# Kernel optimization log

Hardware: AMD Instinct MI355X
Metric: run time of the kernel (lower is better)

Reference implementation:

```python
import jax, jax.numpy as jnp
import numpy as np

N, NFEAT, NHID, NCLASS, NLAYERS = 4096, 512, 512, 40, 3
NEG = -9e15


def _adj(key, p=0.01):
    # sparse binary adjacency with self-loops, matching the `adj > 0` masking
    a = (jax.random.uniform(key, (N, N)) < p).astype(jnp.float32)
    return jnp.minimum(a + jnp.eye(N, dtype=jnp.float32), 1.0)


def setup_inputs() -> dict:
    key = jax.random.key(0)
    ks = jax.random.split(key, 16)
    inp = {
        "x": jax.random.normal(ks[0], (N, NFEAT), jnp.float32),
        "adj_att": _adj(ks[1]),
        "adj1": _adj(ks[2]),
        "adj2": _adj(ks[3]),
        "hop_select": jnp.ones((NLAYERS,), jnp.float32),
    }
    s1 = 1.0 / np.sqrt(NFEAT)
    s2 = 1.0 / np.sqrt(NHID)
    for i in range(NLAYERS):
        inp[f"W_fc{i}"] = jax.random.uniform(ks[4 + i], (NFEAT, NHID), jnp.float32, -s1, s1)
        inp[f"b_fc{i}"] = jnp.zeros((NHID,), jnp.float32)
    for i in range(NLAYERS - 1):
        inp[f"W_q{i}"] = jax.random.uniform(ks[7 + 2 * i], (NHID, NHID), jnp.float32, -s2, s2)
        inp[f"b_q{i}"] = jnp.zeros((NHID,), jnp.float32)
        inp[f"W_k{i}"] = jax.random.uniform(ks[8 + 2 * i], (NHID, NHID), jnp.float32, -s2, s2)
        inp[f"b_k{i}"] = jnp.zeros((NHID,), jnp.float32)
    s3 = 1.0 / np.sqrt(NHID * NLAYERS)
    inp["W_cls"] = jax.random.uniform(ks[11], (NHID * NLAYERS, NCLASS), jnp.float32, -s3, s3)
    inp["b_cls"] = jnp.zeros((NCLASS,), jnp.float32)
    return inp


def _gatv3_forward(x, adj_att, adj1, adj2, hop_select,
                   W_fc0, b_fc0, W_fc1, b_fc1, W_fc2, b_fc2,
                   W_q0, b_q0, W_k0, b_k0, W_q1, b_q1, W_k1, b_k1,
                   W_cls, b_cls):
    mask = jax.nn.softmax(hop_select, axis=-1)
    adjs = [None, adj1, adj2]
    fc = [(W_fc0, b_fc0), (W_fc1, b_fc1), (W_fc2, b_fc2)]
    qk = [(W_q0, b_q0, W_k0, b_k0), (W_q1, b_q1, W_k1, b_k1)]
    outs = []
    tmp_1 = None
    for i in range(NLAYERS):
        W, b = fc[i]
        tmp = x @ W + b  # [N, nhid]
        if adjs[i] is not None:
            adj = adjs[i]
            Wq, bq, Wk, bk = qk[i - 1]
            t_att = adj_att @ tmp                      # [N, nhid]
            Q = adj_att @ (t_att @ Wq + bq)            # GCN1 Q, act=None
            K = adj_att @ (t_att @ Wk + bk)            # GCN1 K, act=None
            scores = jnp.where(adj > 0, Q @ K.T, NEG)  # masked QK^T
            att = jax.nn.softmax(scores, axis=-1)
            tmp_1 = jnp.where(adj > 0, att, 0.0)
            tmp = att @ tmp
        # F.normalize(p=2, dim=1) with eps=1e-12 clamp
        nrm = jnp.maximum(jnp.sqrt(jnp.sum(tmp * tmp, axis=1, keepdims=True)), 1e-12)
        outs.append(mask[i] * (tmp / nrm))
    final = jnp.concatenate(outs, axis=1)          # [N, 3*nhid]
    out = jax.nn.relu(final)                       # dropout is identity in eval
    logits = out @ W_cls + b_cls
    return jax.nn.log_softmax(logits, axis=1), tmp_1


def reference(x, adj_att, adj1, adj2, hop_select,
              W_fc0, b_fc0, W_fc1, b_fc1, W_fc2, b_fc2,
              W_q0, b_q0, W_k0, b_k0, W_q1, b_q1, W_k1, b_k1,
              W_cls, b_cls):
    return _gatv3_forward(x, adj_att, adj1, adj2, hop_select,
                          W_fc0, b_fc0, W_fc1, b_fc1, W_fc2, b_fc2,
                          W_q0, b_q0, W_k0, b_k0, W_q1, b_q1, W_k1, b_k1,
                          W_cls, b_cls)
```

## Files before the change

### kernel.cpp

```cpp
#include <hip/hip_runtime.h>
#include <math.h>

#define NN 4096
#define DD 512
#define ELL 128

typedef unsigned long long u64;
typedef __attribute__((ext_vector_type(8))) short short8;
typedef __attribute__((ext_vector_type(8))) unsigned short ushort8;
typedef __attribute__((ext_vector_type(4))) float f32x4;

static __device__ __forceinline__ unsigned short f2bf(float f) {
  unsigned u = __float_as_uint(f);
  unsigned r = (u + 0x7fffu + ((u >> 16) & 1u)) >> 16;
  return (unsigned short)r;
}
static __device__ __forceinline__ float bf2f(unsigned short h) {
  return __uint_as_float(((unsigned)h) << 16);
}

struct Build3 {
  const float *adj0, *adj1, *adj2;
  int *c0, *c1, *c2;
  int *n0, *n1, *n2;
};

__global__ __launch_bounds__(256) void k_build3(Build3 p) {
  const int s = blockIdx.y;
  const float* adj = s == 0 ? p.adj0 : (s == 1 ? p.adj1 : p.adj2);
  int* cols = s == 0 ? p.c0 : (s == 1 ? p.c1 : p.c2);
  int* cnt  = s == 0 ? p.n0 : (s == 1 ? p.n1 : p.n2);
  const int wv = threadIdx.x >> 6;
  const int lane = threadIdx.x & 63;
  const int r = blockIdx.x * 4 + wv;
  const float* row = adj + (size_t)r * NN;
  int* rc = cols + (size_t)r * ELL;
  int base = 0;
  for (int c0 = 0; c0 < NN; c0 += 256) {
    float4 v = *(const float4*)(row + c0 + lane * 4);
    u64 m0 = __ballot(v.x > 0.f);
    u64 m1 = __ballot(v.y > 0.f);
    u64 m2 = __ballot(v.z > 0.f);
    u64 m3 = __ballot(v.w > 0.f);
    u64 below = (1ull << lane) - 1ull;
    int pre = base + __popcll(m0 & below) + __popcll(m1 & below) +
              __popcll(m2 & below) + __popcll(m3 & below);
    int own = 0;
    const int cb = c0 + 4 * lane;
    if (v.x > 0.f) { int id = pre + own; if (id < ELL) rc[id] = cb + 0; own++; }
    if (v.y > 0.f) { int id = pre + own; if (id < ELL) rc[id] = cb + 1; own++; }
    if (v.z > 0.f) { int id = pre + own; if (id < ELL) rc[id] = cb + 2; own++; }
    if (v.w > 0.f) { int id = pre + own; if (id < ELL) rc[id] = cb + 3; own++; }
    base += __popcll(m0) + __popcll(m1) + __popcll(m2) + __popcll(m3);
  }
  if (lane == 0) cnt[r] = base < ELL ? base : ELL;
}

struct SplitE { const float* src; unsigned short* dst; int rows; int bstyle; };
struct Split4 { SplitE e[4]; };

__global__ __launch_bounds__(256) void k_split(Split4 p) {
  SplitE e = p.e[blockIdx.y];
  if (!e.src) return;
  const int oct = blockIdx.x * 256 + threadIdx.x;
  if (oct >= e.rows * 64) return;
  float v[8];
  size_t toff;
  if (!e.bstyle) {
    const int m = oct >> 6, kg = oct & 63;
    const float* sp = e.src + (size_t)m * 512 + kg * 8;
    float4 u0 = *(const float4*)sp;
    float4 u1 = *(const float4*)(sp + 4);
    v[0] = u0.x; v[1] = u0.y; v[2] = u0.z; v[3] = u0.w;
    v[4] = u1.x; v[5] = u1.y; v[6] = u1.z; v[7] = u1.w;
    toff = ((size_t)(m >> 7) * 16 + (kg >> 2)) * 4096 +
           (size_t)((m & 127) >> 4) * 512 + (size_t)(kg & 3) * 128 +
           (size_t)(m & 15) * 8;
  } else {
    const int n = oct & 511, kog = oct >> 9;
    const int k0 = kog * 8;
#pragma unroll
    for (int i = 0; i < 8; i++) v[i] = e.src[(size_t)(k0 + i) * 512 + n];
    toff = ((size_t)(n >> 7) * 16 + (kog >> 2)) * 4096 +
           (size_t)((n & 127) >> 4) * 512 + (size_t)(kog & 3) * 128 +
           (size_t)(n & 15) * 8;
  }
  ushort8 h0, h1, h2;
#pragma unroll
  for (int i = 0; i < 8; i++) {
    float f = v[i];
    unsigned short a0 = f2bf(f);
    float r1 = f - bf2f(a0);
    unsigned short a1 = f2bf(r1);
    float r2 = r1 - bf2f(a1);
    unsigned short a2 = f2bf(r2);
    h0[i] = a0; h1[i] = a1; h2[i] = a2;
  }
  const size_t stride = (size_t)e.rows * 512;
  *(ushort8*)(e.dst + toff) = h0;
  *(ushort8*)(e.dst + stride + toff) = h1;
  *(ushort8*)(e.dst + 2 * stride + toff) = h2;
}

struct ToBf {
  const float *s0, *s1;
  unsigned short *d0, *d1;
};

__global__ __launch_bounds__(256) void k_tobf16(ToBf p) {
  const float* s = blockIdx.y ? p.s1 : p.s0;
  unsigned short* d = blockIdx.y ? p.d1 : p.d0;
  const size_t i = ((size_t)blockIdx.x * 256 + threadIdx.x) * 8;
  float4 a = *(const float4*)(s + i);
  float4 b = *(const float4*)(s + i + 4);
  ushort8 h;
  h[0] = f2bf(a.x); h[1] = f2bf(a.y); h[2] = f2bf(a.z); h[3] = f2bf(a.w);
  h[4] = f2bf(b.x); h[5] = f2bf(b.y); h[6] = f2bf(b.z); h[7] = f2bf(b.w);
  *(ushort8*)(d + i) = h;
}

struct GmP {
  const unsigned short *A0, *A1, *A2;
  const unsigned short *B0, *B1, *B2;
  const float *b0, *b1, *b2;
  float *C0, *C1, *C2;
  size_t sA, sB;
};

#define MMTERM(sa)                                                          \
  _Pragma("unroll")                                                         \
  for (int mi = 0; mi < 4; mi++) {                                          \
    _Pragma("unroll")                                                       \
    for (int ni = 0; ni < 4; ni++)                                          \
      acc[mi][ni] = __builtin_amdgcn_mfma_f32_16x16x32_bf16(                \
          af[sa][mi], bf[ni], acc[mi][ni], 0, 0, 0);                        \
  }

__global__ __launch_bounds__(256) void k_gemm_mfma(GmP p) {
  __shared__ __align__(16) unsigned short Al[3][4096];
  __shared__ __align__(16) unsigned short Bl[3][4096];
  const int tid = threadIdx.x;
  const int mat = blockIdx.y >> 2;
  const int nb = blockIdx.y & 3;
  const int mb = blockIdx.x;
  const unsigned short* A = mat == 0 ? p.A0 : (mat == 1 ? p.A1 : p.A2);
  const unsigned short* B = mat == 0 ? p.B0 : (mat == 1 ? p.B1 : p.B2);
  const float* bias = mat == 0 ? p.b0 : (mat == 1 ? p.b1 : p.b2);
  float* C = mat == 0 ? p.C0 : (mat == 1 ? p.C1 : p.C2);
  const int lane = tid & 63, w = tid >> 6, wr = w >> 1, wc = w & 1;
  const size_t s8A = p.sA >> 3, s8B = p.sB >> 3;

  f32x4 acc[4][4];
#pragma unroll
  for (int mi = 0; mi < 4; mi++)
#pragma unroll
    for (int ni = 0; ni < 4; ni++) acc[mi][ni] = (f32x4){0.f, 0.f, 0.f, 0.f};

  for (int kb = 0; kb < 16; kb++) {
    const short8* ga = (const short8*)(A + ((size_t)mb * 16 + kb) * 4096);
    const short8* gb = (const short8*)(B + ((size_t)nb * 16 + kb) * 4096);
    __syncthreads();
#pragma unroll
    for (int s = 0; s < 3; s++) {
#pragma unroll
      for (int c = 0; c < 2; c++) {
        const int o = tid + c * 256;
        ((short8*)Al[s])[o] = ga[(size_t)s * s8A + o];
        ((short8*)Bl[s])[o] = gb[(size_t)s * s8B + o];
      }
    }
    __syncthreads();
    short8 af[3][4];
#pragma unroll
    for (int s = 0; s < 3; s++)
#pragma unroll
      for (int mi = 0; mi < 4; mi++)
        af[s][mi] = ((const short8*)Al[s])[(wr * 4 + mi) * 64 + lane];
    short8 bf[4];
#pragma unroll
    for (int ni = 0; ni < 4; ni++)
      bf[ni] = ((const short8*)Bl[0])[(wc * 4 + ni) * 64 + lane];
    MMTERM(0) MMTERM(1) MMTERM(2)
#pragma unroll
    for (int ni = 0; ni < 4; ni++)
      bf[ni] = ((const short8*)Bl[1])[(wc * 4 + ni) * 64 + lane];
    MMTERM(0) MMTERM(1)
#pragma unroll
    for (int ni = 0; ni < 4; ni++)
      bf[ni] = ((const short8*)Bl[2])[(wc * 4 + ni) * 64 + lane];
    MMTERM(0)
  }

  const int m0 = mb * 128 + wr * 64;
  const int n0c = nb * 128 + wc * 64 + (lane & 15);
  const int r0 = (lane >> 4) * 4;
#pragma unroll
  for (int mi = 0; mi < 4; mi++) {
#pragma unroll
    for (int ni = 0; ni < 4; ni++) {
      const int col = n0c + ni * 16;
      const float bb = bias ? bias[col] : 0.f;
      f32x4 a = acc[mi][ni];
#pragma unroll
      for (int r = 0; r < 4; r++)
        C[(size_t)(m0 + mi * 16 + r0 + r) * DD + col] = a[r] + bb;
    }
  }
}

struct GemmNT {
  const float *A0, *B0, *A1, *B1;
  float *C0, *C1;
};

__global__ __launch_bounds__(256) void k_gemm_nt(GemmNT p) {
  __shared__ __align__(16) float As[32][68];
  __shared__ __align__(16) float Bs[32][68];
  const int tid = threadIdx.x;
  const int mat = blockIdx.y >> 3;
  const int n0 = (blockIdx.y & 7) * 64;
  const int m0 = blockIdx.x * 64;
  const float* A = mat == 0 ? p.A0 : p.A1;
  const float* B = mat == 0 ? p.B0 : p.B1;
  float* C       = mat == 0 ? p.C0 : p.C1;
  const int tx = tid & 15, ty = tid >> 4;
  const int lr = tid >> 3, lc = (tid & 7) * 4;

  float4 fa[2], fb[2];
#pragma unroll
  for (int q = 0; q < 2; q++) {
    fa[q] = *(const float4*)(A + (size_t)(m0 + lr + 32 * q) * DD + lc);
    fb[q] = *(const float4*)(B + (size_t)(n0 + lr + 32 * q) * DD + lc);
  }
#pragma unroll
  for (int q = 0; q < 2; q++) {
    As[lc + 0][lr + 32 * q] = fa[q].x;
    As[lc + 1][lr + 32 * q] = fa[q].y;
    As[lc + 2][lr + 32 * q] = fa[q].z;
    As[lc + 3][lr + 32 * q] = fa[q].w;
    Bs[lc + 0][lr + 32 * q] = fb[q].x;
    Bs[lc + 1][lr + 32 * q] = fb[q].y;
    Bs[lc + 2][lr + 32 * q] = fb[q].z;
    Bs[lc + 3][lr + 32 * q] = fb[q].w;
  }
  __syncthreads();

  float acc[4][4];
#pragma unroll
  for (int i = 0; i < 4; i++)
#pragma unroll
    for (int j = 0; j < 4; j++) acc[i][j] = 0.f;

  for (int t = 0; t < 16; t++) {
    if (t < 15) {
      const int k0 = (t + 1) * 32;
#pragma unroll
      for (int q = 0; q < 2; q++) {
        fa[q] = *(const float4*)(A + (size_t)(m0 + lr + 32 * q) * DD + k0 + lc);
        fb[q] = *(const float4*)(B + (size_t)(n0 + lr + 32 * q) * DD + k0 + lc);
      }
    }
#pragma unroll
    for (int kk = 0; kk < 32; kk++) {
      float4 a = *(const float4*)&As[kk][ty * 4];
      float4 b = *(const float4*)&Bs[kk][tx * 4];
      float av[4] = {a.x, a.y, a.z, a.w};
      float bv[4] = {b.x, b.y, b.z, b.w};
#pragma unroll
      for (int i = 0; i < 4; i++)
#pragma unroll
        for (int j = 0; j < 4; j++) acc[i][j] = fmaf(av[i], bv[j], acc[i][j]);
    }
    __syncthreads();
    if (t < 15) {
#pragma unroll
      for (int q = 0; q < 2; q++) {
        As[lc + 0][lr + 32 * q] = fa[q].x;
        As[lc + 1][lr + 32 * q] = fa[q].y;
        As[lc + 2][lr + 32 * q] = fa[q].z;
        As[lc + 3][lr + 32 * q] = fa[q].w;
        Bs[lc + 0][lr + 32 * q] = fb[q].x;
        Bs[lc + 1][lr + 32 * q] = fb[q].y;
        Bs[lc + 2][lr + 32 * q] = fb[q].z;
        Bs[lc + 3][lr + 32 * q] = fb[q].w;
      }
      __syncthreads();
    }
  }

#pragma unroll
  for (int i = 0; i < 4; i++) {
    const int m = m0 + ty * 4 + i;
    float4 o = {acc[i][0], acc[i][1], acc[i][2], acc[i][3]};
    *(float4*)(C + (size_t)m * DD + n0 + tx * 4) = o;
  }
}

struct W12P {
  const float *Wq0, *bk0, *Wk0, *bq0;
  const float *Wq1, *bk1, *Wk1, *bq1;
  float *w10, *w20, *w11, *w21, *gam;
};

__global__ __launch_bounds__(256) void k_w12(W12P p) {
  const int l = blockIdx.y;
  const float* Wq = l ? p.Wq1 : p.Wq0;
  const float* bk = l ? p.bk1 : p.bk0;
  const float* Wk = l ? p.Wk1 : p.Wk0;
  const float* bq = l ? p.bq1 : p.bq0;
  float* w1 = l ? p.w11 : p.w10;
  float* w2 = l ? p.w21 : p.w20;
  const int wv = threadIdx.x >> 6, lane = threadIdx.x & 63;
  const int r = blockIdx.x * 4 + wv;
  float s1 = 0.f, s2 = 0.f;
  for (int k = lane; k < DD; k += 64) {
    s1 = fmaf(Wq[(size_t)r * DD + k], bk[k], s1);
    s2 = fmaf(Wk[(size_t)r * DD + k], bq[k], s2);
  }
#pragma unroll
  for (int off = 32; off > 0; off >>= 1) {
    s1 += __shfl_xor(s1, off);
    s2 += __shfl_xor(s2, off);
  }
  if (lane == 0) { w1[r] = s1; w2[r] = s2; }
  if (blockIdx.x == 0 && wv == 0) {
    float g = 0.f;
    for (int k = lane; k < DD; k += 64) g = fmaf(bq[k], bk[k], g);
#pragma unroll
    for (int off = 32; off > 0; off >>= 1) g += __shfl_xor(g, off);
    if (lane == 0) p.gam[l] = g;
  }
}

struct AbP {
  const float *U1, *U2, *w10, *w20, *w11, *w21;
  float *a1, *b1, *a2, *b2;
};

__global__ __launch_bounds__(256) void k_ab(AbP p) {
  const int wv = threadIdx.x >> 6, lane = threadIdx.x & 63;
  const int r = blockIdx.x * 4 + wv;
  const int base = lane * 8;
  float4 wa0 = *(const float4*)(p.w10 + base);
  float4 wa1 = *(const float4*)(p.w10 + base + 4);
  float4 wb0 = *(const float4*)(p.w20 + base);
  float4 wb1 = *(const float4*)(p.w20 + base + 4);
  float4 u0 = *(const float4*)(p.U1 + (size_t)r * DD + base);
  float4 u1 = *(const float4*)(p.U1 + (size_t)r * DD + base + 4);
  float sa = u0.x * wa0.x + u0.y * wa0.y + u0.z * wa0.z + u0.w * wa0.w +
             u1.x * wa1.x + u1.y * wa1.y + u1.z * wa1.z + u1.w * wa1.w;
  float sb = u0.x * wb0.x + u0.y * wb0.y + u0.z * wb0.z + u0.w * wb0.w +
             u1.x * wb1.x + u1.y * wb1.y + u1.z * wb1.z + u1.w * wb1.w;
#pragma unroll
  for (int off = 32; off > 0; off >>= 1) {
    sa += __shfl_xor(sa, off);
    sb += __shfl_xor(sb, off);
  }
  if (lane == 0) { p.a1[r] = sa; p.b1[r] = sb; }
  wa0 = *(const float4*)(p.w11 + base);
  wa1 = *(const float4*)(p.w11 + base + 4);
  wb0 = *(const float4*)(p.w21 + base);
  wb1 = *(const float4*)(p.w21 + base + 4);
  u0 = *(const float4*)(p.U2 + (size_t)r * DD + base);
  u1 = *(const float4*)(p.U2 + (size_t)r * DD + base + 4);
  sa = u0.x * wa0.x + u0.y * wa0.y + u0.z * wa0.z + u0.w * wa0.w +
       u1.x * wa1.x + u1.y * wa1.y + u1.z * wa1.z + u1.w * wa1.w;
  sb = u0.x * wb0.x + u0.y * wb0.y + u0.z * wb0.z + u0.w * wb0.w +
       u1.x * wb1.x + u1.y * wb1.y + u1.z * wb1.z + u1.w * wb1.w;
#pragma unroll
  for (int off = 32; off > 0; off >>= 1) {
    sa += __shfl_xor(sa, off);
    sb += __shfl_xor(sb, off);
  }
  if (lane == 0) { p.a2[r] = sa; p.b2[r] = sb; }
}

struct Sd2 {
  const int *cols0, *cnts0, *cols1, *cnts1;
  const float *V0, *U0, *al0, *be0;
  const unsigned short *T0;
  const float *V1, *U1, *al1, *be1;
  const unsigned short *T1;
  const float* gam;
  const int* degA;
  float *out0, *out1, *dense;
};

__global__ __launch_bounds__(256) void k_sddmm_out(Sd2 p) {
  const int l = blockIdx.y;
  const int* cols = l ? p.cols1 : p.cols0;
  const int* cnts = l ? p.cnts1 : p.cnts0;
  const float* V = l ? p.V1 : p.V0;
  const float* U = l ? p.U1 : p.U0;
  const float* al = l ? p.al1 : p.al0;
  const float* be = l ? p.be1 : p.be0;
  const unsigned short* Tb = l ? p.T1 : p.T0;
  float* out = l ? p.out1 : p.out0;
  float* dense = l ? p.dense : nullptr;
  const int r = blockIdx.x;
  const int t = threadIdx.x;
  const int lane = t & 63, wv = t >> 6;
  const int cnt = cnts[r];
  __shared__ int scol[ELL];
  __shared__ float ssc[ELL];
  if (t < ELL) scol[t] = (t < cnt) ? cols[(size_t)r * ELL + t] : 0;
  if (dense) {
    float4 z = {0.f, 0.f, 0.f, 0.f};
    float4* drow = (float4*)(dense + (size_t)r * NN);
#pragma unroll
    for (int q = 0; q < 4; q++) drow[t + 256 * q] = z;
  }
  __syncthreads();
  const float g = p.gam[l];
  const float dr = (float)p.degA[r];
  const float ar = al[r];
  const float* Vr = V + (size_t)r * DD + lane * 8;
  float4 q0 = *(const float4*)Vr;
  float4 q1 = *(const float4*)(Vr + 4);
  for (int k = wv; k < cnt; k += 4) {
    const int c = scol[k];
    const float* Uc = U + (size_t)c * DD + lane * 8;
    float4 k0 = *(const float4*)Uc;
    float4 k1 = *(const float4*)(Uc + 4);
    float s = q0.x * k0.x + q0.y * k0.y + q0.z * k0.z + q0.w * k0.w +
              q1.x * k1.x + q1.y * k1.y + q1.z * k1.z + q1.w * k1.w;
#pragma unroll
    for (int off = 32; off > 0; off >>= 1) s += __shfl_xor(s, off);
    if (lane == 0) {
      const float dc = (float)p.degA[c];
      ssc[k] = s + dc * ar + dr * be[c] + dr * dc * g;
    }
  }
  __syncthreads();
  if (wv == 0) {
    float v0 = (lane < cnt) ? ssc[lane] : -INFINITY;
    float v1 = (lane + 64 < cnt) ? ssc[lane + 64] : -INFINITY;
    float mx = fmaxf(v0, v1);
#pragma unroll
    for (int off = 32; off > 0; off >>= 1) mx = fmaxf(mx, __shfl_xor(mx, off));
    float e0 = (lane < cnt) ? expf(v0 - mx) : 0.f;
    float e1 = (lane + 64 < cnt) ? expf(v1 - mx) : 0.f;
    float sm = e0 + e1;
#pragma unroll
    for (int off = 32; off > 0; off >>= 1) sm += __shfl_xor(sm, off);
    float inv = 1.f / sm;
    if (lane < cnt) ssc[lane] = e0 * inv;
    if (lane + 64 < cnt) ssc[lane + 64] = e1 * inv;
  }
  __syncthreads();
  if (t < cnt && dense) dense[(size_t)r * NN + scol[t]] = ssc[t];
  float a0 = 0.f, a1 = 0.f;
#pragma unroll 4
  for (int k = 0; k < cnt; k++) {
    const float v = ssc[k];
    const unsigned u = *(const unsigned*)(Tb + (size_t)scol[k] * DD + t * 2);
    a0 = fmaf(v, __uint_as_float(u << 16), a0);
    a1 = fmaf(v, __uint_as_float(u & 0xffff0000u), a1);
  }
  float2 o = {a0, a1};
  *(float2*)(out + (size_t)r * DD + t * 2) = o;
}

struct SpF {
  const int *colsA, *cntsA, *colsB, *cntsB;
  const float *BA, *BB;
  float *CA, *CB;
};

__global__ __launch_bounds__(256) void k_spmm_f4(SpF p) {
  const int mat = blockIdx.y;
  const int* cols = mat ? p.colsB : p.colsA;
  const int* cnts = mat ? p.cntsB : p.cntsA;
  const float* B = mat ? p.BB : p.BA;
  float* C = mat ? p.CB : p.CA;
  const int hr = threadIdx.x >> 7;
  const int j = threadIdx.x & 127;
  const int row = blockIdx.x * 2 + hr;
  __shared__ int scol[2][ELL];
  const int cnt = cnts[row];
  scol[hr][j] = (j < cnt) ? cols[(size_t)row * ELL + j] : 0;
  __syncthreads();
  float4 acc = {0.f, 0.f, 0.f, 0.f};
#pragma unroll 4
  for (int k = 0; k < cnt; k++) {
    float4 b = *(const float4*)(B + (size_t)scol[hr][k] * DD + j * 4);
    acc.x += b.x; acc.y += b.y; acc.z += b.z; acc.w += b.w;
  }
  *(float4*)(C + (size_t)row * DD + j * 4) = acc;
}

__global__ __launch_bounds__(256) void k_norm_cls(const float* __restrict__ T0,
                                                  const float* __restrict__ T1,
                                                  const float* __restrict__ T2,
                                                  const float* __restrict__ hop,
                                                  const float* __restrict__ Wc,
                                                  const float* __restrict__ bc,
                                                  float* __restrict__ out) {
  const int r = blockIdx.x;
  const int t = threadIdx.x;
  const int lane = t & 63, wv = t >> 6;
  __shared__ __align__(16) float srow[1536];
  __shared__ float red[4];
  __shared__ float pr[6][40];
  float h0 = hop[0], h1 = hop[1], h2 = hop[2];
  float hm = fmaxf(h0, fmaxf(h1, h2));
  float e0 = expf(h0 - hm), e1 = expf(h1 - hm), e2 = expf(h2 - hm);
  float minv = 1.f / (e0 + e1 + e2);
  float mask[3] = {e0 * minv, e1 * minv, e2 * minv};
  const float* Ts[3] = {T0, T1, T2};
#pragma unroll
  for (int s = 0; s < 3; s++) {
    float x0 = Ts[s][(size_t)r * DD + t];
    float x1 = Ts[s][(size_t)r * DD + t + 256];
    float ss = x0 * x0 + x1 * x1;
#pragma unroll
    for (int off = 32; off > 0; off >>= 1) ss += __shfl_xor(ss, off);
    if (lane == 0) red[wv] = ss;
    __syncthreads();
    float tot = red[0] + red[1] + red[2] + red[3];
    float nrm = fmaxf(sqrtf(tot), 1e-12f);
    float sc = mask[s] / nrm;
    srow[s * DD + t] = fmaxf(x0 * sc, 0.f);
    srow[s * DD + t + 256] = fmaxf(x1 * sc, 0.f);
    __syncthreads();
  }
  float part = 0.f;
  const int col = t % 40, seg = t / 40;
  if (seg < 6) {
    const float* w = Wc + col;
#pragma unroll 4
    for (int k = seg * 256; k < seg * 256 + 256; k++)
      part = fmaf(srow[k], w[(size_t)k * 40], part);
    pr[seg][col] = part;
  }
  __syncthreads();
  if (t < 64) {
    float lg = -INFINITY;
    if (t < 40) {
      lg = bc[t];
#pragma unroll
      for (int s6 = 0; s6 < 6; s6++) lg += pr[s6][t];
    }
    float mx = lg;
#pragma unroll
    for (int off = 32; off > 0; off >>= 1) mx = fmaxf(mx, __shfl_xor(mx, off));
    float ex = (t < 40) ? expf(lg - mx) : 0.f;
    float sm = ex;
#pragma unroll
    for (int off = 32; off > 0; off >>= 1) sm += __shfl_xor(sm, off);
    float ls = logf(sm);
    if (t < 40) out[(size_t)r * 40 + t] = lg - mx - ls;
  }
}

extern "C" void kernel_launch(void* const* d_in, const int* in_sizes, int n_in,
                              void* d_out, int out_size, void* d_ws, size_t ws_size,
                              hipStream_t stream) {
  (void)in_sizes; (void)n_in; (void)out_size; (void)ws_size;
  const float* x    = (const float*)d_in[0];
  const float* adjA = (const float*)d_in[1];
  const float* adj1 = (const float*)d_in[2];
  const float* adj2 = (const float*)d_in[3];
  const float* hop  = (const float*)d_in[4];
  const float* Wfc0 = (const float*)d_in[5];  const float* bfc0 = (const float*)d_in[6];
  const float* Wfc1 = (const float*)d_in[7];  const float* bfc1 = (const float*)d_in[8];
  const float* Wfc2 = (const float*)d_in[9];  const float* bfc2 = (const float*)d_in[10];
  const float* Wq0  = (const float*)d_in[11]; const float* bq0  = (const float*)d_in[12];
  const float* Wk0  = (const float*)d_in[13]; const float* bk0  = (const float*)d_in[14];
  const float* Wq1  = (const float*)d_in[15]; const float* bq1  = (const float*)d_in[16];
  const float* Wk1  = (const float*)d_in[17]; const float* bk1  = (const float*)d_in[18];
  const float* Wc   = (const float*)d_in[19]; const float* bc   = (const float*)d_in[20];

  float* ws = (float*)d_ws;
  const size_t MD = (size_t)NN * DD;
  const size_t WD = (size_t)DD * DD;
  float* TMP0 = ws + 0 * MD;
  float* TMP1 = ws + 1 * MD;
  float* TMP2 = ws + 2 * MD;
  float* S3   = ws + 3 * MD;
  float* S4   = ws + 4 * MD;
  float* U1   = ws + 5 * MD;
  float* U2   = ws + 6 * MD;
  float* M1   = ws + 7 * MD;
  float* M2   = M1 + WD;
  float* w10 = M2 + WD;
  float* w20 = w10 + DD;
  float* w11 = w20 + DD;
  float* w21 = w11 + DD;
  float* gam = w21 + DD;
  float* AL1 = gam + 4;
  float* BE1 = AL1 + NN;
  float* AL2 = BE1 + NN;
  float* BE2 = AL2 + NN;
  int* ELLA = (int*)(BE2 + NN);
  int* ELL1 = ELLA + (size_t)NN * ELL;
  int* ELL2 = ELL1 + (size_t)NN * ELL;
  int* CNTA = ELL2 + (size_t)NN * ELL;
  int* CNT1 = CNTA + NN;
  int* CNT2 = CNT1 + NN;
  unsigned short* Tb1 = (unsigned short*)(CNT2 + NN);
  unsigned short* Tb2 = Tb1 + MD;

  float* outLog = (float*)d_out;
  float* outAtt = outLog + (size_t)NN * 40;
  unsigned short* xb   = (unsigned short*)outAtt;
  unsigned short* wfcb = xb + 3 * MD;
  unsigned short* Ub1  = wfcb + 9 * WD;
  unsigned short* Ub2  = Ub1 + 3 * MD;
  unsigned short* Mb1  = Ub2 + 3 * MD;
  unsigned short* Mb2  = Mb1 + 3 * WD;

  Build3 pb{adjA, adj1, adj2, ELLA, ELL1, ELL2, CNTA, CNT1, CNT2};
  k_build3<<<dim3(NN / 4, 3), 256, 0, stream>>>(pb);

  W12P pw{Wq0, bk0, Wk0, bq0, Wq1, bk1, Wk1, bq1, w10, w20, w11, w21, gam};
  k_w12<<<dim3(DD / 4, 2), 256, 0, stream>>>(pw);

  Split4 sp1{{{x, xb, NN, 0},
              {Wfc0, wfcb + 0 * 3 * WD, DD, 1},
              {Wfc1, wfcb + 1 * 3 * WD, DD, 1},
              {Wfc2, wfcb + 2 * 3 * WD, DD, 1}}};
  k_split<<<dim3(1024, 4), 256, 0, stream>>>(sp1);

  GmP pf{xb, xb, xb,
         wfcb + 0 * 3 * WD, wfcb + 1 * 3 * WD, wfcb + 2 * 3 * WD,
         bfc0, bfc1, bfc2, TMP0, TMP1, TMP2, MD, WD};
  k_gemm_mfma<<<dim3(32, 12), 256, 0, stream>>>(pf);

  GemmNT pm{Wq0, Wk0, Wq1, Wk1, M1, M2};
  k_gemm_nt<<<dim3(8, 16), 256, 0, stream>>>(pm);

  ToBf tb{TMP1, TMP2, Tb1, Tb2};
  k_tobf16<<<dim3(1024, 2), 256, 0, stream>>>(tb);

  SpF s1{ELLA, CNTA, ELLA, CNTA, TMP1, TMP2, S3, S4};
  k_spmm_f4<<<dim3(NN / 2, 2), 256, 0, stream>>>(s1);
  SpF s2{ELLA, CNTA, ELLA, CNTA, S3, S4, U1, U2};
  k_spmm_f4<<<dim3(NN / 2, 2), 256, 0, stream>>>(s2);

  Split4 sp2{{{U1, Ub1, NN, 0},
              {U2, Ub2, NN, 0},
              {M1, Mb1, DD, 1},
              {M2, Mb2, DD, 1}}};
  k_split<<<dim3(1024, 4), 256, 0, stream>>>(sp2);

  GmP pv{Ub1, Ub2, nullptr, Mb1, Mb2, nullptr,
         nullptr, nullptr, nullptr, S3, S4, nullptr, MD, WD};
  k_gemm_mfma<<<dim3(32, 8), 256, 0, stream>>>(pv);

  AbP pab{U1, U2, w10, w20, w11, w21, AL1, BE1, AL2, BE2};
  k_ab<<<NN / 4, 256, 0, stream>>>(pab);

  Sd2 sd{ELL1, CNT1, ELL2, CNT2,
         S3, U1, AL1, BE1, Tb1,
         S4, U2, AL2, BE2, Tb2,
         gam, CNTA, S3, S4, outAtt};
  k_sddmm_out<<<dim3(NN, 2), 256, 0, stream>>>(sd);

  k_norm_cls<<<NN, 256, 0, stream>>>(TMP0, S3, S4, hop, Wc, bc, outLog);
}
```

Before: 439.1 us.

## Fuse bf16 conversion into GEMM epilogue, merge SpMM rows, prefetch loads

The separate fp32-to-bf16 conversion kernel is removed, and the first MFMA GEMM now writes bf16 copies of TMP1 and TMP2 in its epilogue. The SpMM kernel now has one block handle the same row for both matrices, so the column indices are loaded once. The adjacency build loads all sixteen float4 chunks up front to raise memory-level parallelism. The SDDMM score loop software-prefetches the next neighbor's U row. The costs are more registers in the build kernel and scattered 2-byte stores in the GEMM epilogue.

```diff
diff --git a/kernel.cpp b/kernel.cpp
--- a/kernel.cpp
+++ b/kernel.cpp
@@ -35,22 +35,26 @@
   const int r = blockIdx.x * 4 + wv;
   const float* row = adj + (size_t)r * NN;
   int* rc = cols + (size_t)r * ELL;
+  float4 v[16];
+#pragma unroll
+  for (int i = 0; i < 16; i++)
+    v[i] = *(const float4*)(row + i * 256 + lane * 4);
   int base = 0;
-  for (int c0 = 0; c0 < NN; c0 += 256) {
-    float4 v = *(const float4*)(row + c0 + lane * 4);
-    u64 m0 = __ballot(v.x > 0.f);
-    u64 m1 = __ballot(v.y > 0.f);
-    u64 m2 = __ballot(v.z > 0.f);
-    u64 m3 = __ballot(v.w > 0.f);
-    u64 below = (1ull << lane) - 1ull;
+  const u64 below = (1ull << lane) - 1ull;
+#pragma unroll
+  for (int i = 0; i < 16; i++) {
+    u64 m0 = __ballot(v[i].x > 0.f);
+    u64 m1 = __ballot(v[i].y > 0.f);
+    u64 m2 = __ballot(v[i].z > 0.f);
+    u64 m3 = __ballot(v[i].w > 0.f);
     int pre = base + __popcll(m0 & below) + __popcll(m1 & below) +
               __popcll(m2 & below) + __popcll(m3 & below);
     int own = 0;
-    const int cb = c0 + 4 * lane;
-    if (v.x > 0.f) { int id = pre + own; if (id < ELL) rc[id] = cb + 0; own++; }
-    if (v.y > 0.f) { int id = pre + own; if (id < ELL) rc[id] = cb + 1; own++; }
-    if (v.z > 0.f) { int id = pre + own; if (id < ELL) rc[id] = cb + 2; own++; }
-    if (v.w > 0.f) { int id = pre + own; if (id < ELL) rc[id] = cb + 3; own++; }
+    const int cb = i * 256 + 4 * lane;
+    if (v[i].x > 0.f) { int id = pre + own; if (id < ELL) rc[id] = cb + 0; own++; }
+    if (v[i].y > 0.f) { int id = pre + own; if (id < ELL) rc[id] = cb + 1; own++; }
+    if (v[i].z > 0.f) { int id = pre + own; if (id < ELL) rc[id] = cb + 2; own++; }
+    if (v[i].w > 0.f) { int id = pre + own; if (id < ELL) rc[id] = cb + 3; own++; }
     base += __popcll(m0) + __popcll(m1) + __popcll(m2) + __popcll(m3);
   }
   if (lane == 0) cnt[r] = base < ELL ? base : ELL;
@@ -102,28 +106,12 @@
   *(ushort8*)(e.dst + 2 * stride + toff) = h2;
 }
 
-struct ToBf {
-  const float *s0, *s1;
-  unsigned short *d0, *d1;
-};
-
-__global__ __launch_bounds__(256) void k_tobf16(ToBf p) {
-  const float* s = blockIdx.y ? p.s1 : p.s0;
-  unsigned short* d = blockIdx.y ? p.d1 : p.d0;
-  const size_t i = ((size_t)blockIdx.x * 256 + threadIdx.x) * 8;
-  float4 a = *(const float4*)(s + i);
-  float4 b = *(const float4*)(s + i + 4);
-  ushort8 h;
-  h[0] = f2bf(a.x); h[1] = f2bf(a.y); h[2] = f2bf(a.z); h[3] = f2bf(a.w);
-  h[4] = f2bf(b.x); h[5] = f2bf(b.y); h[6] = f2bf(b.z); h[7] = f2bf(b.w);
-  *(ushort8*)(d + i) = h;
-}
-
 struct GmP {
   const unsigned short *A0, *A1, *A2;
   const unsigned short *B0, *B1, *B2;
   const float *b0, *b1, *b2;
   float *C0, *C1, *C2;
+  unsigned short *Cb0, *Cb1, *Cb2;
   size_t sA, sB;
 };
 
@@ -147,6 +135,7 @@
   const unsigned short* B = mat == 0 ? p.B0 : (mat == 1 ? p.B1 : p.B2);
   const float* bias = mat == 0 ? p.b0 : (mat == 1 ? p.b1 : p.b2);
   float* C = mat == 0 ? p.C0 : (mat == 1 ? p.C1 : p.C2);
+  unsigned short* Cb = mat == 0 ? p.Cb0 : (mat == 1 ? p.Cb1 : p.Cb2);
   const int lane = tid & 63, w = tid >> 6, wr = w >> 1, wc = w & 1;
   const size_t s8A = p.sA >> 3, s8B = p.sB >> 3;
 
@@ -202,8 +191,12 @@
       const float bb = bias ? bias[col] : 0.f;
       f32x4 a = acc[mi][ni];
 #pragma unroll
-      for (int r = 0; r < 4; r++)
-        C[(size_t)(m0 + mi * 16 + r0 + r) * DD + col] = a[r] + bb;
+      for (int r = 0; r < 4; r++) {
+        const size_t idx = (size_t)(m0 + mi * 16 + r0 + r) * DD + col;
+        const float val = a[r] + bb;
+        C[idx] = val;
+        if (Cb) Cb[idx] = f2bf(val);
+      }
     }
   }
 }
@@ -417,19 +410,32 @@
   const float* Vr = V + (size_t)r * DD + lane * 8;
   float4 q0 = *(const float4*)Vr;
   float4 q1 = *(const float4*)(Vr + 4);
-  for (int k = wv; k < cnt; k += 4) {
-    const int c = scol[k];
-    const float* Uc = U + (size_t)c * DD + lane * 8;
-    float4 k0 = *(const float4*)Uc;
-    float4 k1 = *(const float4*)(Uc + 4);
-    float s = q0.x * k0.x + q0.y * k0.y + q0.z * k0.z + q0.w * k0.w +
-              q1.x * k1.x + q1.y * k1.y + q1.z * k1.z + q1.w * k1.w;
+  int k = wv;
+  float4 c0, c1;
+  if (k < cnt) {
+    const float* Uc = U + (size_t)scol[k] * DD + lane * 8;
+    c0 = *(const float4*)Uc;
+    c1 = *(const float4*)(Uc + 4);
+  }
+  while (k < cnt) {
+    const int kn = k + 4;
+    float4 n0, n1;
+    if (kn < cnt) {
+      const float* Un = U + (size_t)scol[kn] * DD + lane * 8;
+      n0 = *(const float4*)Un;
+      n1 = *(const float4*)(Un + 4);
+    }
+    float s = q0.x * c0.x + q0.y * c0.y + q0.z * c0.z + q0.w * c0.w +
+              q1.x * c1.x + q1.y * c1.y + q1.z * c1.z + q1.w * c1.w;
 #pragma unroll
     for (int off = 32; off > 0; off >>= 1) s += __shfl_xor(s, off);
     if (lane == 0) {
+      const int c = scol[k];
       const float dc = (float)p.degA[c];
       ssc[k] = s + dc * ar + dr * be[c] + dr * dc * g;
     }
+    c0 = n0; c1 = n1;
+    k = kn;
   }
   __syncthreads();
   if (wv == 0) {
@@ -451,9 +457,9 @@
   if (t < cnt && dense) dense[(size_t)r * NN + scol[t]] = ssc[t];
   float a0 = 0.f, a1 = 0.f;
 #pragma unroll 4
-  for (int k = 0; k < cnt; k++) {
-    const float v = ssc[k];
-    const unsigned u = *(const unsigned*)(Tb + (size_t)scol[k] * DD + t * 2);
+  for (int kk = 0; kk < cnt; kk++) {
+    const float v = ssc[kk];
+    const unsigned u = *(const unsigned*)(Tb + (size_t)scol[kk] * DD + t * 2);
     a0 = fmaf(v, __uint_as_float(u << 16), a0);
     a1 = fmaf(v, __uint_as_float(u & 0xffff0000u), a1);
   }
@@ -461,32 +467,30 @@
   *(float2*)(out + (size_t)r * DD + t * 2) = o;
 }
 
-struct SpF {
-  const int *colsA, *cntsA, *colsB, *cntsB;
-  const float *BA, *BB;
-  float *CA, *CB;
+struct Sp2 {
+  const int *cols, *cnts;
+  const float *B1, *B2;
+  float *C1, *C2;
 };
 
-__global__ __launch_bounds__(256) void k_spmm_f4(SpF p) {
-  const int mat = blockIdx.y;
-  const int* cols = mat ? p.colsB : p.colsA;
-  const int* cnts = mat ? p.cntsB : p.cntsA;
-  const float* B = mat ? p.BB : p.BA;
-  float* C = mat ? p.CB : p.CA;
-  const int hr = threadIdx.x >> 7;
+__global__ __launch_bounds__(256) void k_spmm2(Sp2 p) {
+  const int r = blockIdx.x;
+  const int half = threadIdx.x >> 7;
   const int j = threadIdx.x & 127;
-  const int row = blockIdx.x * 2 + hr;
-  __shared__ int scol[2][ELL];
-  const int cnt = cnts[row];
-  scol[hr][j] = (j < cnt) ? cols[(size_t)row * ELL + j] : 0;
+  const float* B = half ? p.B2 : p.B1;
+  float* C = half ? p.C2 : p.C1;
+  __shared__ int scol[ELL];
+  const int cnt = p.cnts[r];
+  if (threadIdx.x < ELL)
+    scol[threadIdx.x] = (threadIdx.x < cnt) ? p.cols[(size_t)r * ELL + threadIdx.x] : 0;
   __syncthreads();
   float4 acc = {0.f, 0.f, 0.f, 0.f};
 #pragma unroll 4
   for (int k = 0; k < cnt; k++) {
-    float4 b = *(const float4*)(B + (size_t)scol[hr][k] * DD + j * 4);
+    float4 b = *(const float4*)(B + (size_t)scol[k] * DD + j * 4);
     acc.x += b.x; acc.y += b.y; acc.z += b.z; acc.w += b.w;
   }
-  *(float4*)(C + (size_t)row * DD + j * 4) = acc;
+  *(float4*)(C + (size_t)r * DD + j * 4) = acc;
 }
 
 __global__ __launch_bounds__(256) void k_norm_cls(const float* __restrict__ T0,
@@ -624,19 +628,17 @@
 
   GmP pf{xb, xb, xb,
          wfcb + 0 * 3 * WD, wfcb + 1 * 3 * WD, wfcb + 2 * 3 * WD,
-         bfc0, bfc1, bfc2, TMP0, TMP1, TMP2, MD, WD};
+         bfc0, bfc1, bfc2, TMP0, TMP1, TMP2,
+         nullptr, Tb1, Tb2, MD, WD};
   k_gemm_mfma<<<dim3(32, 12), 256, 0, stream>>>(pf);
 
   GemmNT pm{Wq0, Wk0, Wq1, Wk1, M1, M2};
   k_gemm_nt<<<dim3(8, 16), 256, 0, stream>>>(pm);
 
-  ToBf tb{TMP1, TMP2, Tb1, Tb2};
-  k_tobf16<<<dim3(1024, 2), 256, 0, stream>>>(tb);
-
-  SpF s1{ELLA, CNTA, ELLA, CNTA, TMP1, TMP2, S3, S4};
-  k_spmm_f4<<<dim3(NN / 2, 2), 256, 0, stream>>>(s1);
-  SpF s2{ELLA, CNTA, ELLA, CNTA, S3, S4, U1, U2};
-  k_spmm_f4<<<dim3(NN / 2, 2), 256, 0, stream>>>(s2);
+  Sp2 s1{ELLA, CNTA, TMP1, TMP2, S3, S4};
+  k_spmm2<<<NN, 256, 0, stream>>>(s1);
+  Sp2 s2{ELLA, CNTA, S3, S4, U1, U2};
+  k_spmm2<<<NN, 256, 0, stream>>>(s2);
 
   Split4 sp2{{{U1, Ub1, NN, 0},
               {U2, Ub2, NN, 0},
@@ -645,7 +647,8 @@
   k_split<<<dim3(1024, 4), 256, 0, stream>>>(sp2);
 
   GmP pv{Ub1, Ub2, nullptr, Mb1, Mb2, nullptr,
-         nullptr, nullptr, nullptr, S3, S4, nullptr, MD, WD};
+         nullptr, nullptr, nullptr, S3, S4, nullptr,
+         nullptr, nullptr, nullptr, MD, WD};
   k_gemm_mfma<<<dim3(32, 8), 256, 0, stream>>>(pv);
 
   AbP pab{U1, U2, w10, w20, w11, w21, AL1, BE1, AL2, BE2};
```

Result: slower. 488.2 us (+11.2%).
